# Performance work log

Measured on AMD Instinct MI355X. Metric: run time of the kernel, lower is better.

Reference implementation:

```python
import jax, jax.numpy as jnp
import numpy as np

B, T, E, H = 2, 4096, 1024, 16
SEGS = (256, 512, 1024, 2048, 4096)
DILS = (1, 2, 4, 8, 16)
NEG = -1e8  # torchscale uses -1e8 for uncovered / masked lse entries


def setup_inputs() -> dict:
    key = jax.random.key(0)
    ks = jax.random.split(key, 5)
    sc = 0.02
    zb = jnp.zeros((E,), jnp.float32)
    return {
        "x": jax.random.normal(ks[0], (B, T, E), jnp.float32),
        "wq": jax.random.normal(ks[1], (E, E), jnp.float32) * sc,
        "bq": zb,
        "wk": jax.random.normal(ks[2], (E, E), jnp.float32) * sc,
        "bk": zb,
        "wv": jax.random.normal(ks[3], (E, E), jnp.float32) * sc,
        "bv": zb,
        "wo": jax.random.normal(ks[4], (E, E), jnp.float32) * sc,
        "bo": zb,
    }


def _scale_attn(q, k, v, w, r):
    # One LongNet scale: segment length w, dilation ratio r.
    # Head group g = head // (H//r) attends to in-segment positions p with p % r == g
    # (torchscale dense_to_sparse diagonal over (r1, r2)).
    Bq, Tq, Hq, d = q.shape
    n, s, hp = Tq // w, w // r, Hq // r  # segments, sparse length, heads per group

    def gather(x):
        # [B,T,H,d] -> segments [B,n,w,H,d]; split w=(s,r1) (p=l*r+r1) and H=(r2,hp);
        # keep diagonal r1 == r2.
        x = x.reshape(Bq, n, s, r, r, hp, d)
        x = jnp.diagonal(x, axis1=3, axis2=4)          # [B,n,s,hp,d,r]
        return jnp.moveaxis(x, -1, 3).reshape(Bq, n, s, Hq, d)

    qs, ks_, vs = gather(q), gather(k), gather(v)
    scores = jnp.einsum('bnqhd,bnkhd->bnhqk', qs, ks_)
    mask = jnp.tril(jnp.ones((s, s), dtype=bool))       # causal within sparse segment
    scores = jnp.where(mask, scores, NEG)
    lse = jax.scipy.special.logsumexp(scores, axis=-1)  # [B,n,h,q]
    out = jnp.einsum('bnhqk,bnkhd->bnqhd', jax.nn.softmax(scores, axis=-1), vs)

    # Scatter back to dense positions (sparse_to_dense): uncovered -> out 0, lse -1e8.
    eye = jnp.eye(r, dtype=out.dtype)
    out_g = out.reshape(Bq, n, s, r, hp, d)                               # heads as (g, hp)
    dense = jnp.einsum('bnsghd,pg->bnspghd', out_g, eye).reshape(Bq, Tq, Hq, d)
    lse_g = jnp.transpose(lse, (0, 1, 3, 2)).reshape(Bq, n, s, r, hp)     # [B,n,s,g,hp]
    lse_d = jnp.where(eye[:, :, None] > 0, lse_g[:, :, :, None, :, :], NEG)
    return dense, lse_d.reshape(Bq, Tq, Hq)


def reference(x, wq, bq, wk, bk, wv, bv, wo, bo):
    d = E // H
    q = (x @ wq + bq).reshape(B, T, H, d) * (d ** -0.5)
    k = (x @ wk + bk).reshape(B, T, H, d)
    v = (x @ wv + bv).reshape(B, T, H, d)
    outs, lses = [], []
    for w_, r_ in zip(SEGS, DILS):
        o, l = _scale_attn(q, k, v, w_, r_)
        outs.append(o)
        lses.append(l)
    # Merge scales with softmax over per-scale log-sum-exp (dense-attention equivalence).
    wgt = jax.nn.softmax(jnp.stack(lses), axis=0)[..., None]  # [S,B,T,H,1]
    y = jnp.sum(jnp.stack(outs) * wgt, axis=0).reshape(B, T, E)
    return y @ wo + bo
```

## Files before the change

### kernel.cpp

```cpp
#include <hip/hip_runtime.h>
#include <hip/hip_bf16.h>

typedef __bf16 bf16_t;
typedef __bf16 bf16x8 __attribute__((ext_vector_type(8)));
typedef __bf16 bf16x4 __attribute__((ext_vector_type(4)));
typedef float f32x4 __attribute__((ext_vector_type(4)));
typedef int vint4 __attribute__((ext_vector_type(4)));

constexpr int B_ = 2, T_ = 4096, E_ = 1024, H_ = 16;
constexpr int M_ = B_ * T_;

__device__ constexpr size_t OB_OFF[5]  = {0, 8388608, 12582912, 14680064, 15728640};
__device__ constexpr size_t LSE_OFF[5] = {0, 131072, 196608, 229376, 245760};
constexpr size_t OB_TOTAL  = 16252928;
constexpr size_t LSE_TOTAL = 253952;

__global__ __launch_bounds__(256) void cvt_f32_bf16(const float* __restrict__ in,
                                                    bf16_t* __restrict__ out) {
  int i = (blockIdx.x * 256 + threadIdx.x) * 4;
  const float4 v = *(const float4*)(in + i);
  bf16x4 o;
  o[0] = (bf16_t)v.x; o[1] = (bf16_t)v.y; o[2] = (bf16_t)v.z; o[3] = (bf16_t)v.w;
  *(bf16x4*)(out + i) = o;
}

__global__ __launch_bounds__(256) void cvt_transpose_w(
    const float* __restrict__ w0, const float* __restrict__ w1,
    const float* __restrict__ w2, const float* __restrict__ w3,
    bf16_t* __restrict__ o0, bf16_t* __restrict__ o1,
    bf16_t* __restrict__ o2, bf16_t* __restrict__ o3) {
  __shared__ float tile[32][33];
  const float* src; bf16_t* dst;
  switch (blockIdx.z) {
    case 0: src = w0; dst = o0; break;
    case 1: src = w1; dst = o1; break;
    case 2: src = w2; dst = o2; break;
    default: src = w3; dst = o3; break;
  }
  const int n0 = blockIdx.x * 32, k0 = blockIdx.y * 32;
  const int tx = threadIdx.x & 31, ty = threadIdx.x >> 5;
#pragma unroll
  for (int i = 0; i < 32; i += 8)
    tile[ty + i][tx] = src[(size_t)(k0 + ty + i) * E_ + n0 + tx];
  __syncthreads();
#pragma unroll
  for (int i = 0; i < 32; i += 8)
    dst[(size_t)(n0 + ty + i) * E_ + k0 + tx] = (bf16_t)tile[tx][ty + i];
}

#define BM 128
#define BN 128
#define BKg 64

template <bool OUT_BF16, bool QKV>
__global__ __launch_bounds__(256, 2) void gemm_bt(
    const bf16_t* __restrict__ A, const bf16_t* __restrict__ BT,
    const float* __restrict__ bias0, const float* __restrict__ bias1,
    const float* __restrict__ bias2, void* __restrict__ Cout, int Kdim) {
  __shared__ bf16_t As[BM * BKg];
  __shared__ bf16_t Bs[BN * BKg];
  const int tid = threadIdx.x;
  const int lane = tid & 63;
  const int wave = tid >> 6;
  const int wm = wave >> 1, wn = wave & 1;
  const int bm = blockIdx.x;
  int bn = blockIdx.y;

  const float* bias = bias0;
  float scale = 1.0f;
  void* outp = Cout;
  if (QKV) {
    const int which = bn >> 3;
    bn &= 7;
    bias = (which == 0) ? bias0 : (which == 1) ? bias1 : bias2;
    scale = (which == 0) ? 0.125f : 1.0f;
    outp = (void*)((bf16_t*)Cout + (size_t)which * M_ * E_);
    BT += (size_t)which * E_ * E_;
  }

  f32x4 acc[4][4] = {};

  const int lrow = tid >> 3;
  const int lcol = (tid & 7) * 8;
  const bf16_t* Ag = A + (size_t)(bm * BM + lrow) * Kdim + lcol;
  const bf16_t* Bg = BT + (size_t)(bn * BN + lrow) * Kdim + lcol;
  bf16_t* Asd = &As[lrow * BKg + lcol];
  bf16_t* Bsd = &Bs[lrow * BKg + lcol];

  for (int k0 = 0; k0 < Kdim; k0 += BKg) {
    __syncthreads();
#pragma unroll
    for (int j = 0; j < 4; ++j) {
      __builtin_amdgcn_global_load_lds(
          (const __attribute__((address_space(1))) void*)(Ag + (size_t)(j * 32) * Kdim + k0),
          (__attribute__((address_space(3))) void*)(Asd + j * 32 * BKg), 16, 0, 0);
      __builtin_amdgcn_global_load_lds(
          (const __attribute__((address_space(1))) void*)(Bg + (size_t)(j * 32) * Kdim + k0),
          (__attribute__((address_space(3))) void*)(Bsd + j * 32 * BKg), 16, 0, 0);
    }
    __syncthreads();
#pragma unroll
    for (int kk = 0; kk < 2; ++kk) {
      bf16x8 af[4], bfr[4];
#pragma unroll
      for (int i = 0; i < 4; ++i) {
        af[i]  = *(const bf16x8*)&As[(wm * 64 + i * 16 + (lane & 15)) * BKg + kk * 32 + (lane >> 4) * 8];
        bfr[i] = *(const bf16x8*)&Bs[(wn * 64 + i * 16 + (lane & 15)) * BKg + kk * 32 + (lane >> 4) * 8];
      }
#pragma unroll
      for (int i = 0; i < 4; ++i)
#pragma unroll
        for (int j = 0; j < 4; ++j)
          acc[i][j] = __builtin_amdgcn_mfma_f32_16x16x32_bf16(af[i], bfr[j], acc[i][j], 0, 0, 0);
    }
  }

#pragma unroll
  for (int i = 0; i < 4; ++i) {
    const int row = bm * BM + wm * 64 + i * 16 + (lane >> 4) * 4;
#pragma unroll
    for (int j = 0; j < 4; ++j) {
      const int col = bn * BN + wn * 64 + j * 16 + (lane & 15);
      const float bv = bias[col];
#pragma unroll
      for (int rg = 0; rg < 4; ++rg) {
        const float v = (acc[i][j][rg] + bv) * scale;
        if (OUT_BF16)
          ((bf16_t*)outp)[(size_t)(row + rg) * E_ + col] = (bf16_t)v;
        else
          ((float*)outp)[(size_t)(row + rg) * E_ + col] = v;
      }
    }
  }
}

__global__ __launch_bounds__(512, 4) void attn_inst(
    const bf16_t* __restrict__ Q, const bf16_t* __restrict__ K,
    const bf16_t* __restrict__ V, bf16_t* __restrict__ Ob,
    float* __restrict__ Lse) {
  __shared__ alignas(16) bf16_t Ks[256][72];
  __shared__ alignas(16) bf16_t Vt[64][264];
  __shared__ alignas(16) bf16_t Pw[8][16][40];

  const int bid = blockIdx.x;
  int s, ibase;
  if (bid < 512)      { s = 0; ibase = 0; }
  else if (bid < 768) { s = 1; ibase = 512; }
  else if (bid < 896) { s = 2; ibase = 768; }
  else if (bid < 960) { s = 3; ibase = 896; }
  else                { s = 4; ibase = 960; }
  const int inst = bid - ibase;
  const int h = inst & 15;
  const int nseg_log = 4 - s;
  const int seg = (inst >> 4) & ((1 << nseg_log) - 1);
  const int b = inst >> (4 + nseg_log);
  const int g = h >> (4 - s);

  const int t = threadIdx.x;
  const int lane = t & 63;
  const int wv = t >> 6;
  const int lc = lane & 15;
  const int lg = lane >> 4;

  {
    const int row = t >> 1, ch = (t & 1) * 32;
    const int tk = ((seg * 256 + row) << s) + g;
    const size_t off = ((size_t)b * T_ + tk) * E_ + h * 64 + ch;
    const bf16_t* Kg = K + off;
    const bf16_t* Vg = V + off;
#pragma unroll
    for (int j = 0; j < 4; ++j)
      *(bf16x8*)&Ks[row][ch + j * 8] = *(const bf16x8*)(Kg + j * 8);
#pragma unroll
    for (int j = 0; j < 4; ++j) {
      bf16x8 va = *(const bf16x8*)(Vg + j * 8);
#pragma unroll
      for (int e = 0; e < 8; ++e) Vt[ch + j * 8 + e][row] = va[e];
    }
  }
  __syncthreads();

  const size_t rowbase = (size_t)(b * H_ + h) * (T_ >> s) + seg * 256;

#pragma unroll
  for (int sel = 0; sel < 2; ++sel) {
    const int tile = sel ? (15 - wv) : wv;
    const int q = tile * 16 + lc;

    const int tq = ((seg * 256 + q) << s) + g;
    const bf16_t* Qg = Q + ((size_t)b * T_ + tq) * E_ + h * 64 + lg * 8;
    bf16x8 qfrag0 = *(const bf16x8*)(Qg);
    bf16x8 qfrag1 = *(const bf16x8*)(Qg + 32);

    float m = -INFINITY, Z = 0.0f;
    f32x4 Oa[4] = {};

    const int nkb = tile / 2 + 1;
    const int diag = tile / 2;
    for (int kb = 0; kb < nkb; ++kb) {
      f32x4 sacc[2] = {};
      __builtin_amdgcn_s_setprio(1);
#pragma unroll
      for (int kt = 0; kt < 2; ++kt) {
        bf16x8 kf0 = *(const bf16x8*)&Ks[kb * 32 + kt * 16 + lc][lg * 8];
        bf16x8 kf1 = *(const bf16x8*)&Ks[kb * 32 + kt * 16 + lc][32 + lg * 8];
        sacc[kt] = __builtin_amdgcn_mfma_f32_16x16x32_bf16(kf0, qfrag0, sacc[kt], 0, 0, 0);
        sacc[kt] = __builtin_amdgcn_mfma_f32_16x16x32_bf16(kf1, qfrag1, sacc[kt], 0, 0, 0);
      }
      __builtin_amdgcn_s_setprio(0);
      if (kb == diag) {
#pragma unroll
        for (int kt = 0; kt < 2; ++kt)
#pragma unroll
          for (int rg = 0; rg < 4; ++rg)
            if (kb * 32 + kt * 16 + lg * 4 + rg > q) sacc[kt][rg] = -1e30f;
      }
      float pm = fmaxf(fmaxf(fmaxf(sacc[0][0], sacc[0][1]), fmaxf(sacc[0][2], sacc[0][3])),
                       fmaxf(fmaxf(sacc[1][0], sacc[1][1]), fmaxf(sacc[1][2], sacc[1][3])));
      pm = fmaxf(pm, __shfl_xor(pm, 16));
      pm = fmaxf(pm, __shfl_xor(pm, 32));
      const float nm = fmaxf(m, pm);
      const float crr = __expf(m - nm);
      m = nm;
      float psum = 0.0f;
#pragma unroll
      for (int kt = 0; kt < 2; ++kt)
#pragma unroll
        for (int rg = 0; rg < 4; ++rg) {
          const float p = __expf(sacc[kt][rg] - nm);
          psum += p;
          Pw[wv][lc][kt * 16 + lg * 4 + rg] = (bf16_t)p;
        }
      psum += __shfl_xor(psum, 16);
      psum += __shfl_xor(psum, 32);
      Z = Z * crr + psum;
#pragma unroll
      for (int dt = 0; dt < 4; ++dt)
#pragma unroll
        for (int rg = 0; rg < 4; ++rg) Oa[dt][rg] *= crr;
      bf16x8 pb = *(const bf16x8*)&Pw[wv][lc][lg * 8];
      __builtin_amdgcn_s_setprio(1);
#pragma unroll
      for (int dt = 0; dt < 4; ++dt) {
        bf16x8 vf = *(const bf16x8*)&Vt[dt * 16 + lc][kb * 32 + lg * 8];
        Oa[dt] = __builtin_amdgcn_mfma_f32_16x16x32_bf16(vf, pb, Oa[dt], 0, 0, 0);
      }
      __builtin_amdgcn_s_setprio(0);
    }

    const float lse = m + __logf(Z);
    const float iZ = 1.0f / Z;
    bf16_t* orow = Ob + OB_OFF[s] + (rowbase + q) * 64 + lg * 4;
#pragma unroll
    for (int dt = 0; dt < 4; ++dt) {
      bf16x4 ov;
      ov[0] = (bf16_t)(Oa[dt][0] * iZ);
      ov[1] = (bf16_t)(Oa[dt][1] * iZ);
      ov[2] = (bf16_t)(Oa[dt][2] * iZ);
      ov[3] = (bf16_t)(Oa[dt][3] * iZ);
      *(bf16x4*)(orow + dt * 16) = ov;
    }
    if (lg == 0) Lse[LSE_OFF[s] + rowbase + q] = lse;
  }
}

__global__ __launch_bounds__(256) void attn_merge(const bf16_t* __restrict__ Ob,
                                                  const float* __restrict__ Lse,
                                                  bf16_t* __restrict__ Y) {
  const int gtid = blockIdx.x * 256 + threadIdx.x;
  const int d8 = gtid & 7;
  const int h = (gtid >> 3) & 15;
  const int tt = (gtid >> 7) & (T_ - 1);
  const int b = gtid >> 19;

  float m = -INFINITY, S = 0.0f;
  float acc[8];
#pragma unroll
  for (int j = 0; j < 8; ++j) acc[j] = 0.0f;

#pragma unroll
  for (int s = 0; s < 5; ++s) {
    const int r = 1 << s;
    const int g = h >> (4 - s);
    if ((tt & (r - 1)) != g) continue;
    const size_t idx = (size_t)(b * H_ + h) * (T_ >> s) + (tt >> s);
    const float lse = Lse[LSE_OFF[s] + idx];
    const bf16x8 ov = *(const bf16x8*)(Ob + OB_OFF[s] + idx * 64 + d8 * 8);
    const float nM = fmaxf(m, lse);
    const float a = __expf(m - nM);
    const float e = __expf(lse - nM);
#pragma unroll
    for (int j = 0; j < 8; ++j) acc[j] = acc[j] * a + (float)ov[j] * e;
    S = S * a + e;
    m = nM;
  }

  const float invS = 1.0f / S;
  bf16x8 o;
#pragma unroll
  for (int j = 0; j < 8; ++j) o[j] = (bf16_t)(acc[j] * invS);
  *(bf16x8*)(Y + (size_t)gtid * 8) = o;
}

extern "C" void kernel_launch(void* const* d_in, const int* in_sizes, int n_in,
                              void* d_out, int out_size, void* d_ws, size_t ws_size,
                              hipStream_t stream) {
  (void)in_sizes; (void)n_in; (void)out_size; (void)ws_size;
  const float* x  = (const float*)d_in[0];
  const float* wq = (const float*)d_in[1];
  const float* bq = (const float*)d_in[2];
  const float* wk = (const float*)d_in[3];
  const float* bk = (const float*)d_in[4];
  const float* wv = (const float*)d_in[5];
  const float* bv = (const float*)d_in[6];
  const float* wo = (const float*)d_in[7];
  const float* bo = (const float*)d_in[8];

  char* p = (char*)d_ws;
  auto take = [&](size_t bytes) {
    char* q = p;
    p += (bytes + 255) & ~(size_t)255;
    return (void*)q;
  };
  bf16_t* wq_t = (bf16_t*)take((size_t)E_ * E_ * 2);
  bf16_t* wk_t = (bf16_t*)take((size_t)E_ * E_ * 2);
  bf16_t* wv_t = (bf16_t*)take((size_t)E_ * E_ * 2);
  bf16_t* wo_t = (bf16_t*)take((size_t)E_ * E_ * 2);
  bf16_t* xb   = (bf16_t*)take((size_t)M_ * E_ * 2);
  bf16_t* qb   = (bf16_t*)take((size_t)M_ * E_ * 2);
  bf16_t* kbuf = (bf16_t*)take((size_t)M_ * E_ * 2);
  bf16_t* vbuf = (bf16_t*)take((size_t)M_ * E_ * 2);
  bf16_t* yb   = (bf16_t*)take((size_t)M_ * E_ * 2);
  bf16_t* Ob   = (bf16_t*)take(OB_TOTAL * 2);
  float*  Lse  = (float*)take(LSE_TOTAL * 4);
  (void)wk_t; (void)wv_t;

  cvt_f32_bf16<<<M_ * E_ / 1024, 256, 0, stream>>>(x, xb);
  cvt_transpose_w<<<dim3(32, 32, 4), 256, 0, stream>>>(wq, wk, wv, wo, wq_t, wk_t, wv_t, wo_t);

  gemm_bt<true, true><<<dim3(M_ / BM, 3 * E_ / BN), 256, 0, stream>>>(
      xb, wq_t, bq, bk, bv, qb, E_);

  attn_inst<<<992, 512, 0, stream>>>(qb, kbuf, vbuf, Ob, Lse);

  attn_merge<<<M_ * E_ / 8 / 256, 256, 0, stream>>>(Ob, Lse, yb);

  gemm_bt<false, false><<<dim3(M_ / BM, E_ / BN), 256, 0, stream>>>(
      yb, wo_t, bo, bo, bo, d_out, E_);
}
```

Baseline: 150.4 us.

## Rewrite projection GEMMs with 128x256 tiles and triple-buffered swizzled LDS pipeline

Replaces the 128x128 single-buffered GEMM with a 512-thread 128x256 tile kernel. It uses a three-stage global_load_lds ring buffer, an XOR-swizzled LDS layout to avoid bank conflicts, and split phases that interleave prefetch with MFMA under raised wave priority. The goal is to hide global load latency and improve operand reuse in the QKV and output projections. In exchange it uses 144KB of LDS, allows one block per CU, and launches fewer blocks (768 for QKV, 256 for output), which may leave CUs underfilled.

```diff
diff --git a/kernel.cpp b/kernel.cpp
--- a/kernel.cpp
+++ b/kernel.cpp
@@ -6,6 +6,9 @@
 typedef __bf16 bf16x4 __attribute__((ext_vector_type(4)));
 typedef float f32x4 __attribute__((ext_vector_type(4)));
 typedef int vint4 __attribute__((ext_vector_type(4)));
+
+#define AS1 __attribute__((address_space(1)))
+#define AS3 __attribute__((address_space(3)))
 
 constexpr int B_ = 2, T_ = 4096, E_ = 1024, H_ = 16;
 constexpr int M_ = B_ * T_;
@@ -48,79 +51,117 @@
     dst[(size_t)(n0 + ty + i) * E_ + k0 + tx] = (bf16_t)tile[tx][ty + i];
 }
 
-#define BM 128
-#define BN 128
-#define BKg 64
-
 template <bool OUT_BF16, bool QKV>
-__global__ __launch_bounds__(256, 2) void gemm_bt(
+__global__ __launch_bounds__(512, 1) void gemm8p(
     const bf16_t* __restrict__ A, const bf16_t* __restrict__ BT,
     const float* __restrict__ bias0, const float* __restrict__ bias1,
-    const float* __restrict__ bias2, void* __restrict__ Cout, int Kdim) {
-  __shared__ bf16_t As[BM * BKg];
-  __shared__ bf16_t Bs[BN * BKg];
+    const float* __restrict__ bias2, void* __restrict__ Cout) {
+  constexpr int K = E_;
+  constexpr int NKT = K / 64;
+  __shared__ bf16_t Sm[73728];
+
   const int tid = threadIdx.x;
   const int lane = tid & 63;
-  const int wave = tid >> 6;
-  const int wm = wave >> 1, wn = wave & 1;
+  const int wid = tid >> 6;
+  const int wm = wid >> 2, wn = wid & 3;
+  const int lc = lane & 15, lg = lane >> 4;
   const int bm = blockIdx.x;
   int bn = blockIdx.y;
 
   const float* bias = bias0;
   float scale = 1.0f;
   void* outp = Cout;
+  const bf16_t* Bt = BT;
   if (QKV) {
-    const int which = bn >> 3;
-    bn &= 7;
+    const int which = bn >> 2;
+    bn &= 3;
     bias = (which == 0) ? bias0 : (which == 1) ? bias1 : bias2;
     scale = (which == 0) ? 0.125f : 1.0f;
     outp = (void*)((bf16_t*)Cout + (size_t)which * M_ * E_);
-    BT += (size_t)which * E_ * E_;
-  }
+    Bt += (size_t)which * E_ * E_;
+  }
+
+  const int srow = tid >> 3;
+  const int schunk = (tid & 7) ^ (srow & 7);
+  const bf16_t* Ag = A + (size_t)(bm * 128 + srow) * K + schunk * 8;
+  const bf16_t* Bg = Bt + (size_t)(bn * 256 + srow) * K + schunk * 8;
+
+  const int sl0 = (lg ^ (lc & 7)) * 8;
+  const int sl1 = ((4 + lg) ^ (lc & 7)) * 8;
 
   f32x4 acc[4][4] = {};
 
-  const int lrow = tid >> 3;
-  const int lcol = (tid & 7) * 8;
-  const bf16_t* Ag = A + (size_t)(bm * BM + lrow) * Kdim + lcol;
-  const bf16_t* Bg = BT + (size_t)(bn * BN + lrow) * Kdim + lcol;
-  bf16_t* Asd = &As[lrow * BKg + lcol];
-  bf16_t* Bsd = &Bs[lrow * BKg + lcol];
-
-  for (int k0 = 0; k0 < Kdim; k0 += BKg) {
-    __syncthreads();
+  auto stA = [&](int kt, int bu, int l) {
+    __builtin_amdgcn_global_load_lds(
+        (const AS1 void*)(Ag + (size_t)(l * 64) * K + kt * 64),
+        (AS3 void*)(Sm + bu * 8192 + l * 4096 + tid * 8), 16, 0, 0);
+  };
+  auto stB = [&](int kt, int bu, int l) {
+    __builtin_amdgcn_global_load_lds(
+        (const AS1 void*)(Bg + (size_t)(l * 64) * K + kt * 64),
+        (AS3 void*)(Sm + 24576 + bu * 16384 + l * 4096 + tid * 8), 16, 0, 0);
+  };
+
+  stA(0, 0, 0); stA(0, 0, 1);
+  stB(0, 0, 0); stB(0, 0, 1); stB(0, 0, 2); stB(0, 0, 3);
+  stA(1, 1, 0); stA(1, 1, 1);
+  stB(1, 1, 0); stB(1, 1, 1); stB(1, 1, 2); stB(1, 1, 3);
+  asm volatile("s_waitcnt vmcnt(6)" ::: "memory");
+  __builtin_amdgcn_s_barrier();
+
+  for (int kt = 0; kt < NKT; ++kt) {
+    const int bc = kt % 3;
+    const int bs = (kt + 2) % 3;
+    const bool st = (kt + 2) < NKT;
+    const int arow = bc * 8192 + (wm * 64 + lc) * 64;
+    const int brow = 24576 + bc * 16384 + (wn * 64 + lc) * 64;
+
+#pragma unroll
+    for (int ph = 0; ph < 2; ++ph) {
+      bf16x8 afr[2][2], bfr[4][2];
+#pragma unroll
+      for (int i2 = 0; i2 < 2; ++i2) {
+        const int rb = arow + (ph * 32 + i2 * 16) * 64;
+        afr[i2][0] = *(const bf16x8*)&Sm[rb + sl0];
+        afr[i2][1] = *(const bf16x8*)&Sm[rb + sl1];
+      }
+#pragma unroll
+      for (int j = 0; j < 4; ++j) {
+        const int rb = brow + j * 16 * 64;
+        bfr[j][0] = *(const bf16x8*)&Sm[rb + sl0];
+        bfr[j][1] = *(const bf16x8*)&Sm[rb + sl1];
+      }
+      if (st) {
+        if (ph == 0) { stA(kt + 2, bs, 0); stB(kt + 2, bs, 0); stB(kt + 2, bs, 1); }
+        else         { stA(kt + 2, bs, 1); stB(kt + 2, bs, 2); stB(kt + 2, bs, 3); }
+      }
+      __builtin_amdgcn_s_barrier();
+      asm volatile("s_waitcnt lgkmcnt(0)" ::: "memory");
+      __builtin_amdgcn_s_setprio(1);
+#pragma unroll
+      for (int i2 = 0; i2 < 2; ++i2)
+#pragma unroll
+        for (int j = 0; j < 4; ++j) {
+          acc[ph * 2 + i2][j] = __builtin_amdgcn_mfma_f32_16x16x32_bf16(
+              afr[i2][0], bfr[j][0], acc[ph * 2 + i2][j], 0, 0, 0);
+          acc[ph * 2 + i2][j] = __builtin_amdgcn_mfma_f32_16x16x32_bf16(
+              afr[i2][1], bfr[j][1], acc[ph * 2 + i2][j], 0, 0, 0);
+        }
+      __builtin_amdgcn_s_setprio(0);
+      if (ph == 1) {
+        if (st) asm volatile("s_waitcnt vmcnt(6)" ::: "memory");
+        else    asm volatile("s_waitcnt vmcnt(0)" ::: "memory");
+      }
+      __builtin_amdgcn_s_barrier();
+    }
+  }
+
+#pragma unroll
+  for (int i = 0; i < 4; ++i) {
+    const int row = bm * 128 + wm * 64 + i * 16 + lg * 4;
 #pragma unroll
     for (int j = 0; j < 4; ++j) {
-      __builtin_amdgcn_global_load_lds(
-          (const __attribute__((address_space(1))) void*)(Ag + (size_t)(j * 32) * Kdim + k0),
-          (__attribute__((address_space(3))) void*)(Asd + j * 32 * BKg), 16, 0, 0);
-      __builtin_amdgcn_global_load_lds(
-          (const __attribute__((address_space(1))) void*)(Bg + (size_t)(j * 32) * Kdim + k0),
-          (__attribute__((address_space(3))) void*)(Bsd + j * 32 * BKg), 16, 0, 0);
-    }
-    __syncthreads();
-#pragma unroll
-    for (int kk = 0; kk < 2; ++kk) {
-      bf16x8 af[4], bfr[4];
-#pragma unroll
-      for (int i = 0; i < 4; ++i) {
-        af[i]  = *(const bf16x8*)&As[(wm * 64 + i * 16 + (lane & 15)) * BKg + kk * 32 + (lane >> 4) * 8];
-        bfr[i] = *(const bf16x8*)&Bs[(wn * 64 + i * 16 + (lane & 15)) * BKg + kk * 32 + (lane >> 4) * 8];
-      }
-#pragma unroll
-      for (int i = 0; i < 4; ++i)
-#pragma unroll
-        for (int j = 0; j < 4; ++j)
-          acc[i][j] = __builtin_amdgcn_mfma_f32_16x16x32_bf16(af[i], bfr[j], acc[i][j], 0, 0, 0);
-    }
-  }
-
-#pragma unroll
-  for (int i = 0; i < 4; ++i) {
-    const int row = bm * BM + wm * 64 + i * 16 + (lane >> 4) * 4;
-#pragma unroll
-    for (int j = 0; j < 4; ++j) {
-      const int col = bn * BN + wn * 64 + j * 16 + (lane & 15);
+      const int col = bn * 256 + wn * 64 + j * 16 + lc;
       const float bv = bias[col];
 #pragma unroll
       for (int rg = 0; rg < 4; ++rg) {
@@ -338,13 +379,13 @@
   cvt_f32_bf16<<<M_ * E_ / 1024, 256, 0, stream>>>(x, xb);
   cvt_transpose_w<<<dim3(32, 32, 4), 256, 0, stream>>>(wq, wk, wv, wo, wq_t, wk_t, wv_t, wo_t);
 
-  gemm_bt<true, true><<<dim3(M_ / BM, 3 * E_ / BN), 256, 0, stream>>>(
-      xb, wq_t, bq, bk, bv, qb, E_);
+  gemm8p<true, true><<<dim3(M_ / 128, 12), 512, 0, stream>>>(
+      xb, wq_t, bq, bk, bv, qb);
 
   attn_inst<<<992, 512, 0, stream>>>(qb, kbuf, vbuf, Ob, Lse);
 
   attn_merge<<<M_ * E_ / 8 / 256, 256, 0, stream>>>(Ob, Lse, yb);
 
-  gemm_bt<false, false><<<dim3(M_ / BM, E_ / BN), 256, 0, stream>>>(
-      yb, wo_t, bo, bo, bo, d_out, E_);
-}
+  gemm8p<false, false><<<dim3(M_ / 128, 4), 512, 0, stream>>>(
+      yb, wo_t, bo, bo, bo, d_out);
+}
```

New measurement: 147.4 us. -2.0%, faster.
